# Optimization experiments

Hardware: AMD Instinct MI355X
Metric: run time of the kernel (lower is better)

## Reference

```python
import jax, jax.numpy as jnp
import numpy as np

N, T, F = 20000, 64, 128          # nodes, time steps, feat_dim
B, K = 8192, 32                   # queries, padded neighbor count
WWIN = 64                         # window_w -> delta table size WWIN+1
DD, MD, HD, HH = 16, 64, 128, 64  # delta_dim, msg_dim, hidden_dim, h_dim
Q = 3 * B                         # (v,s,z) x B node-time aggregations


def _lin(k, i, o):
    k1, k2 = jax.random.split(k)
    w = jax.random.normal(k1, (i, o), jnp.float32) / np.sqrt(i).astype(np.float32)
    b = jax.random.normal(k2, (o,), jnp.float32) * 0.01
    return w, b


def setup_inputs() -> dict:
    key = jax.random.key(0)
    ks = jax.random.split(key, 24)
    x_tensor = jax.random.normal(ks[0], (N, T, F), jnp.float32)
    node_ids = jax.random.randint(ks[1], (Q,), 0, N)
    times = jax.random.randint(ks[2], (Q,), 0, T)
    in_u = jax.random.randint(ks[3], (Q, K), 0, N)
    in_tau = jax.random.randint(ks[4], (Q, K), 0, T)
    in_mask = jax.random.uniform(ks[5], (Q, K)) < 0.5
    out_u = jax.random.randint(ks[6], (Q, K), 0, N)
    out_tau = jax.random.randint(ks[7], (Q, K), 0, T)
    out_mask = jax.random.uniform(ks[8], (Q, K)) < 0.5
    d_norm = jax.random.uniform(ks[9], (B,))
    delta_emb = jax.random.normal(ks[10], (WWIN + 1, DD), jnp.float32) * 0.1
    piw1, pib1 = _lin(ks[11], F + DD, MD)
    piw2, pib2 = _lin(ks[12], MD, MD)
    pow1, pob1 = _lin(ks[13], F + DD, MD)
    pow2, pob2 = _lin(ks[14], MD, MD)
    cw1, cb1 = _lin(ks[15], F + 2 * MD, HD)
    cw2, cb2 = _lin(ks[16], HD, HH)
    sw1, sb1 = _lin(ks[17], 3 * HH + 1, HD)
    sw2, sb2 = _lin(ks[18], HD, 1)
    return dict(x_tensor=x_tensor, d_norm=d_norm, delta_emb=delta_emb,
                piw1=piw1, pib1=pib1, piw2=piw2, pib2=pib2,
                pow1=pow1, pob1=pob1, pow2=pow2, pob2=pob2,
                cw1=cw1, cb1=cb1, cw2=cw2, cb2=cb2,
                sw1=sw1, sb1=sb1, sw2=sw2, sb2=sb2,
                node_ids=node_ids, times=times,
                in_u=in_u, in_tau=in_tau, in_mask=in_mask,
                out_u=out_u, out_tau=out_tau, out_mask=out_mask)


def reference(x_tensor, d_norm, delta_emb,
              piw1, pib1, piw2, pib2,
              pow1, pob1, pow2, pob2,
              cw1, cb1, cw2, cb2,
              sw1, sb1, sw2, sb2,
              node_ids, times, in_u, in_tau, in_mask, out_u, out_tau, out_mask):
    def mlp2(x, w1, b1, w2, b2):  # Linear -> ReLU -> Linear
        return jnp.maximum(x @ w1 + b1, 0.0) @ w2 + b2

    def agg(u, tau, mask, sign, w1, b1, w2, b2):
        # sign=+1: in arcs delta = clamp(t - tau); sign=-1: out arcs delta = clamp(tau - t)
        delta = jnp.clip(sign * (times[:, None] - tau), 0, WWIN)     # [Q,K]
        x_u = x_tensor[u, tau]                                        # [Q,K,F] gather
        msg = mlp2(jnp.concatenate([x_u, delta_emb[delta]], -1), w1, b1, w2, b2)  # [Q,K,MD]
        m = mask[..., None].astype(msg.dtype)
        return (msg * m).sum(1) / jnp.maximum(m.sum(1), 1.0)         # masked mean; empty -> zeros

    m_in = agg(in_u, in_tau, in_mask, 1, piw1, pib1, piw2, pib2)
    m_out = agg(out_u, out_tau, out_mask, -1, pow1, pob1, pow2, pob2)
    x_vt = x_tensor[node_ids, times]                                  # [Q,F]
    # combine: Linear -> ReLU -> (Dropout eval) -> Linear -> ReLU
    h = jnp.maximum(mlp2(jnp.concatenate([x_vt, m_in, m_out], -1), cw1, cb1, cw2, cb2), 0.0)  # [Q,HH]
    feat = jnp.concatenate([h.reshape(B, 3 * HH), d_norm[:, None]], -1)  # [B, 3*HH+1]
    return mlp2(feat, sw1, sb1, sw2, sb2)[:, 0]                       # [B]
```

## Files before the change

kernel.cpp:

```cpp
#include <hip/hip_runtime.h>
#include <hip/hip_bf16.h>

#define NND   20000
#define TSTEP 64
#define FF    128
#define BB    8192
#define KK    32
#define QQ    (3*BB)
#define WWINC 64
#define DDIM  16
#define MDIM  64
#define HDIM  128
#define HHDIM 64

typedef __attribute__((ext_vector_type(8)))  short short8;
typedef __attribute__((ext_vector_type(16))) float f32x16;

union FragU { unsigned u[4]; short8 s; };

static __device__ __forceinline__ unsigned pkbf(float a, float b) {
    union { float f; unsigned u; } ua, ub; ua.f = a; ub.f = b;
    unsigned ra = (ua.u + 0x7FFFu + ((ua.u >> 16) & 1u)) >> 16;
    unsigned rb = (ub.u + 0x7FFFu + ((ub.u >> 16) & 1u)) >> 16;
    return (ra & 0xFFFFu) | (rb << 16);
}
static __device__ __forceinline__ short f2bf(float a) {
    union { float f; unsigned u; } v; v.f = a;
    return (short)((v.u + 0x7FFFu + ((v.u >> 16) & 1u)) >> 16);
}

__global__ void pack_kernel(const float* __restrict__ cw1, const float* __restrict__ cw2,
                            const float* __restrict__ sw1,
                            short* __restrict__ cw1f, short* __restrict__ cw2f,
                            short* __restrict__ sw1f)
{
    const int gid = blockIdx.x * 256 + threadIdx.x;
    const int ln  = gid & 63;
    const int f   = gid >> 6;
    const int kr8 = 8 * (ln >> 5);
    const int c   = ln & 31;
    FragU v;
    if (f < 64) {
        const int s = f >> 2, n = f & 3;
        #pragma unroll
        for (int i = 0; i < 8; i += 2)
            v.u[i >> 1] = pkbf(cw1[(16*s + kr8 + i)     * HDIM + 32*n + c],
                               cw1[(16*s + kr8 + i + 1) * HDIM + 32*n + c]);
        *(short8*)&cw1f[f * 512 + ln * 8] = v.s;
    } else if (f < 80) {
        const int f2 = f - 64, s = f2 >> 1, n = f2 & 1;
        #pragma unroll
        for (int i = 0; i < 8; i += 2)
            v.u[i >> 1] = pkbf(cw2[(16*s + kr8 + i)     * HHDIM + 32*n + c],
                               cw2[(16*s + kr8 + i + 1) * HHDIM + 32*n + c]);
        *(short8*)&cw2f[f2 * 512 + ln * 8] = v.s;
    } else {
        const int f3 = f - 80, s = f3 >> 2, n = f3 & 3;
        #pragma unroll
        for (int i = 0; i < 8; i += 2)
            v.u[i >> 1] = pkbf(sw1[(16*s + kr8 + i)     * HDIM + 32*n + c],
                               sw1[(16*s + kr8 + i + 1) * HDIM + 32*n + c]);
        *(short8*)&sw1f[f3 * 512 + ln * 8] = v.s;
    }
}

#define NW  4
#define HLD 72

__global__ __launch_bounds__(256, 3)
void agg_mfma_kernel(const float* __restrict__ x, const float* __restrict__ demb,
                     const float* __restrict__ w1, const float* __restrict__ b1,
                     const float* __restrict__ w2, const float* __restrict__ b2,
                     const int* __restrict__ times, const int* __restrict__ uu,
                     const int* __restrict__ tt, const int* __restrict__ mm,
                     float* __restrict__ mout, const int sign, const int nwaves)
{
    __shared__ short w1f[9 * 2 * 64 * 8];
    __shared__ short Hs[NW][KK * HLD];

    const int tid  = threadIdx.x;
    const int lane = tid & 63;
    const int wv   = tid >> 6;
    const int r    = lane & 31;
    const int hi   = lane >> 5;

    for (int f = tid; f < 9 * 2 * 64; f += 256) {
        const int ln = f & 63, sn = f >> 6, s = sn >> 1, n = sn & 1;
        const int krow = 16 * s + 8 * (ln >> 5);
        const int col  = 32 * n + (ln & 31);
        #pragma unroll
        for (int i = 0; i < 8; i += 2) {
            const float va = w1[(krow + i) * MDIM + col];
            const float vb = w1[(krow + i + 1) * MDIM + col];
            *(unsigned*)&w1f[f * 8 + i] = pkbf(va, vb);
        }
    }
    short8 w2f[4][2];
    #pragma unroll
    for (int s = 0; s < 4; s++)
        #pragma unroll
        for (int n = 0; n < 2; n++) {
            FragU fu;
            #pragma unroll
            for (int i = 0; i < 8; i += 2) {
                const float va = w2[(16 * s + 8 * hi + i) * MDIM + 32 * n + r];
                const float vb = w2[(16 * s + 8 * hi + i + 1) * MDIM + 32 * n + r];
                fu.u[i >> 1] = pkbf(va, vb);
            }
            w2f[s][n] = fu.s;
        }
    const float b1c0 = b1[r], b1c1 = b1[32 + r];
    const float b2c0 = b2[r], b2c1 = b2[32 + r];
    __syncthreads();

    const int gwave = blockIdx.x * NW + wv;
    for (int q = gwave; q < QQ; q += nwaves) {
        const int t = times[q];
        int xb = 0, db = 0, mk = 0;
        if (lane < KK) {
            const int u   = uu[q * KK + lane];
            const int tau = tt[q * KK + lane];
            mk = mm[q * KK + lane];
            int d = (sign > 0) ? (t - tau) : (tau - t);
            d = d < 0 ? 0 : (d > WWINC ? WWINC : d);
            xb = u * (TSTEP * FF) + tau * FF;
            db = d * DDIM;
        }
        const unsigned long long bal = __ballot(mk != 0);
        const float cnt  = (float)__popcll(bal);
        const float cinv = 1.0f / fmaxf(cnt, 1.0f);
        const float has  = cnt > 0.0f ? 1.0f : 0.0f;
        const int xbr = __shfl(xb, r, 64);
        const int dbr = __shfl(db, r, 64);
        const int mkr = __shfl(mk, r, 64);

        f32x16 acc0, acc1;
        #pragma unroll
        for (int i = 0; i < 16; i++) { acc0[i] = 0.0f; acc1[i] = 0.0f; }

        const float* xrow = x + xbr + 8 * hi;
        #pragma unroll 4
        for (int s = 0; s < 8; s++) {
            float4 p0 = make_float4(0.f, 0.f, 0.f, 0.f), p1 = p0;
            if (mkr) {
                p0 = *(const float4*)(xrow + 16 * s);
                p1 = *(const float4*)(xrow + 16 * s + 4);
            }
            FragU fa;
            fa.u[0] = pkbf(p0.x, p0.y); fa.u[1] = pkbf(p0.z, p0.w);
            fa.u[2] = pkbf(p1.x, p1.y); fa.u[3] = pkbf(p1.z, p1.w);
            const short8 bf0 = *(const short8*)&w1f[(s * 2 + 0) * 512 + lane * 8];
            const short8 bf1 = *(const short8*)&w1f[(s * 2 + 1) * 512 + lane * 8];
            acc0 = __builtin_amdgcn_mfma_f32_32x32x16_bf16(fa.s, bf0, acc0, 0, 0, 0);
            acc1 = __builtin_amdgcn_mfma_f32_32x32x16_bf16(fa.s, bf1, acc1, 0, 0, 0);
        }
        {
            float4 p0 = make_float4(0.f, 0.f, 0.f, 0.f), p1 = p0;
            if (mkr) {
                p0 = *(const float4*)(demb + dbr + 8 * hi);
                p1 = *(const float4*)(demb + dbr + 8 * hi + 4);
            }
            FragU fa;
            fa.u[0] = pkbf(p0.x, p0.y); fa.u[1] = pkbf(p0.z, p0.w);
            fa.u[2] = pkbf(p1.x, p1.y); fa.u[3] = pkbf(p1.z, p1.w);
            const short8 bf0 = *(const short8*)&w1f[(8 * 2 + 0) * 512 + lane * 8];
            const short8 bf1 = *(const short8*)&w1f[(8 * 2 + 1) * 512 + lane * 8];
            acc0 = __builtin_amdgcn_mfma_f32_32x32x16_bf16(fa.s, bf0, acc0, 0, 0, 0);
            acc1 = __builtin_amdgcn_mfma_f32_32x32x16_bf16(fa.s, bf1, acc1, 0, 0, 0);
        }

        #pragma unroll
        for (int g = 0; g < 16; g++) {
            const int rr = (g & 3) + 8 * (g >> 2) + 4 * hi;
            const float mrow = (float)((bal >> rr) & 1ull);
            const float h0 = fmaxf(acc0[g] + b1c0, 0.0f) * mrow;
            const float h1 = fmaxf(acc1[g] + b1c1, 0.0f) * mrow;
            Hs[wv][rr * HLD + r]      = f2bf(h0);
            Hs[wv][rr * HLD + 32 + r] = f2bf(h1);
        }

        f32x16 c0, c1;
        #pragma unroll
        for (int i = 0; i < 16; i++) { c0[i] = 0.0f; c1[i] = 0.0f; }
        #pragma unroll
        for (int s = 0; s < 4; s++) {
            const short8 a = *(const short8*)&Hs[wv][r * HLD + 16 * s + 8 * hi];
            c0 = __builtin_amdgcn_mfma_f32_32x32x16_bf16(a, w2f[s][0], c0, 0, 0, 0);
            c1 = __builtin_amdgcn_mfma_f32_32x32x16_bf16(a, w2f[s][1], c1, 0, 0, 0);
        }

        float p0s = 0.0f, p1s = 0.0f;
        #pragma unroll
        for (int g = 0; g < 16; g++) { p0s += c0[g]; p1s += c1[g]; }
        p0s += __shfl_xor(p0s, 32, 64);
        p1s += __shfl_xor(p1s, 32, 64);
        const float outv = (hi ? p1s : p0s) * cinv + (hi ? b2c1 : b2c0) * has;
        mout[(size_t)q * MDIM + 32 * hi + r] = outv;
    }
}

#define HLD2 136

__global__ __launch_bounds__(64, 2)
void combine_mfma(const float* __restrict__ x,
                  const int* __restrict__ node_ids, const int* __restrict__ times,
                  const float* __restrict__ min_ws, const float* __restrict__ mout_ws,
                  const short* __restrict__ cw1f, const float* __restrict__ cb1,
                  const short* __restrict__ cw2f, const float* __restrict__ cb2,
                  short* __restrict__ h_bf)
{
    __shared__ short Hs[KK * HLD2];
    const int lane = threadIdx.x & 63;
    const int r = lane & 31, hi = lane >> 5;
    const int qb = blockIdx.x * 32;
    const int q  = qb + r;
    const int xb = node_ids[q] * (TSTEP * FF) + times[q] * FF;

    f32x16 acc[4];
    #pragma unroll
    for (int n = 0; n < 4; n++)
        #pragma unroll
        for (int i = 0; i < 16; i++) acc[n][i] = 0.0f;

    const float* xrow = x + xb + 8 * hi;
    #pragma unroll
    for (int s = 0; s < 8; s++) {
        const float4 p0 = *(const float4*)(xrow + 16 * s);
        const float4 p1 = *(const float4*)(xrow + 16 * s + 4);
        FragU fa;
        fa.u[0] = pkbf(p0.x, p0.y); fa.u[1] = pkbf(p0.z, p0.w);
        fa.u[2] = pkbf(p1.x, p1.y); fa.u[3] = pkbf(p1.z, p1.w);
        #pragma unroll
        for (int n = 0; n < 4; n++) {
            const short8 bf = *(const short8*)&cw1f[(s * 4 + n) * 512 + lane * 8];
            acc[n] = __builtin_amdgcn_mfma_f32_32x32x16_bf16(fa.s, bf, acc[n], 0, 0, 0);
        }
    }
    const float* mrow = min_ws + (size_t)q * MDIM + 8 * hi;
    #pragma unroll
    for (int s = 0; s < 4; s++) {
        const float4 p0 = *(const float4*)(mrow + 16 * s);
        const float4 p1 = *(const float4*)(mrow + 16 * s + 4);
        FragU fa;
        fa.u[0] = pkbf(p0.x, p0.y); fa.u[1] = pkbf(p0.z, p0.w);
        fa.u[2] = pkbf(p1.x, p1.y); fa.u[3] = pkbf(p1.z, p1.w);
        #pragma unroll
        for (int n = 0; n < 4; n++) {
            const short8 bf = *(const short8*)&cw1f[((s + 8) * 4 + n) * 512 + lane * 8];
            acc[n] = __builtin_amdgcn_mfma_f32_32x32x16_bf16(fa.s, bf, acc[n], 0, 0, 0);
        }
    }
    const float* orow = mout_ws + (size_t)q * MDIM + 8 * hi;
    #pragma unroll
    for (int s = 0; s < 4; s++) {
        const float4 p0 = *(const float4*)(orow + 16 * s);
        const float4 p1 = *(const float4*)(orow + 16 * s + 4);
        FragU fa;
        fa.u[0] = pkbf(p0.x, p0.y); fa.u[1] = pkbf(p0.z, p0.w);
        fa.u[2] = pkbf(p1.x, p1.y); fa.u[3] = pkbf(p1.z, p1.w);
        #pragma unroll
        for (int n = 0; n < 4; n++) {
            const short8 bf = *(const short8*)&cw1f[((s + 12) * 4 + n) * 512 + lane * 8];
            acc[n] = __builtin_amdgcn_mfma_f32_32x32x16_bf16(fa.s, bf, acc[n], 0, 0, 0);
        }
    }

    #pragma unroll
    for (int n = 0; n < 4; n++) {
        const float bias = cb1[32 * n + r];
        #pragma unroll
        for (int g = 0; g < 16; g++) {
            const int rr = (g & 3) + 8 * (g >> 2) + 4 * hi;
            Hs[rr * HLD2 + 32 * n + r] = f2bf(fmaxf(acc[n][g] + bias, 0.0f));
        }
    }
    __syncthreads();

    f32x16 c0, c1;
    #pragma unroll
    for (int i = 0; i < 16; i++) { c0[i] = 0.0f; c1[i] = 0.0f; }
    #pragma unroll
    for (int s = 0; s < 8; s++) {
        const short8 a = *(const short8*)&Hs[r * HLD2 + 16 * s + 8 * hi];
        const short8 b0 = *(const short8*)&cw2f[(s * 2 + 0) * 512 + lane * 8];
        const short8 b1v = *(const short8*)&cw2f[(s * 2 + 1) * 512 + lane * 8];
        c0 = __builtin_amdgcn_mfma_f32_32x32x16_bf16(a, b0, c0, 0, 0, 0);
        c1 = __builtin_amdgcn_mfma_f32_32x32x16_bf16(a, b1v, c1, 0, 0, 0);
    }
    const float bb0 = cb2[r], bb1 = cb2[32 + r];
    #pragma unroll
    for (int g = 0; g < 16; g++) {
        const int rr = (g & 3) + 8 * (g >> 2) + 4 * hi;
        h_bf[(size_t)(qb + rr) * HHDIM + r]      = f2bf(fmaxf(c0[g] + bb0, 0.0f));
        h_bf[(size_t)(qb + rr) * HHDIM + 32 + r] = f2bf(fmaxf(c1[g] + bb1, 0.0f));
    }
}

__global__ __launch_bounds__(64, 2)
void score_mfma(const short* __restrict__ h_bf, const float* __restrict__ dnorm,
                const short* __restrict__ sw1f, const float* __restrict__ sw1,
                const float* __restrict__ sb1, const float* __restrict__ sw2,
                const float* __restrict__ sb2, float* __restrict__ out)
{
    const int lane = threadIdx.x & 63;
    const int r = lane & 31, hi = lane >> 5;
    const int bb = blockIdx.x * 32;

    f32x16 acc[4];
    #pragma unroll
    for (int n = 0; n < 4; n++)
        #pragma unroll
        for (int i = 0; i < 16; i++) acc[n][i] = 0.0f;

    const short* arow = h_bf + (size_t)(bb + r) * 192 + 8 * hi;
    #pragma unroll
    for (int s = 0; s < 12; s++) {
        const short8 a = *(const short8*)(arow + 16 * s);
        #pragma unroll
        for (int n = 0; n < 4; n++) {
            const short8 bf = *(const short8*)&sw1f[(s * 4 + n) * 512 + lane * 8];
            acc[n] = __builtin_amdgcn_mfma_f32_32x32x16_bf16(a, bf, acc[n], 0, 0, 0);
        }
    }

    float sb1c[4], swr[4], sw2c[4];
    #pragma unroll
    for (int n = 0; n < 4; n++) {
        sb1c[n] = sb1[32 * n + r];
        swr[n]  = sw1[192 * HDIM + 32 * n + r];
        sw2c[n] = sw2[32 * n + r];
    }
    const float sb2v = sb2[0];

    #pragma unroll
    for (int g = 0; g < 16; g++) {
        const int rr = (g & 3) + 8 * (g >> 2) + 4 * hi;
        const float dn = dnorm[bb + rr];
        float p = 0.0f;
        #pragma unroll
        for (int n = 0; n < 4; n++)
            p += fmaxf(acc[n][g] + sb1c[n] + dn * swr[n], 0.0f) * sw2c[n];
        p += __shfl_xor(p, 1);  p += __shfl_xor(p, 2);  p += __shfl_xor(p, 4);
        p += __shfl_xor(p, 8);  p += __shfl_xor(p, 16);
        if (r == 0) out[bb + rr] = p + sb2v;
    }
}

extern "C" void kernel_launch(void* const* d_in, const int* in_sizes, int n_in,
                              void* d_out, int out_size, void* d_ws, size_t ws_size,
                              hipStream_t stream)
{
    const float* x     = (const float*)d_in[0];
    const float* dnorm = (const float*)d_in[1];
    const float* demb  = (const float*)d_in[2];
    const float* piw1  = (const float*)d_in[3];
    const float* pib1  = (const float*)d_in[4];
    const float* piw2  = (const float*)d_in[5];
    const float* pib2  = (const float*)d_in[6];
    const float* pow1  = (const float*)d_in[7];
    const float* pob1  = (const float*)d_in[8];
    const float* pow2  = (const float*)d_in[9];
    const float* pob2  = (const float*)d_in[10];
    const float* cw1   = (const float*)d_in[11];
    const float* cb1   = (const float*)d_in[12];
    const float* cw2   = (const float*)d_in[13];
    const float* cb2   = (const float*)d_in[14];
    const float* sw1   = (const float*)d_in[15];
    const float* sb1   = (const float*)d_in[16];
    const float* sw2   = (const float*)d_in[17];
    const float* sb2   = (const float*)d_in[18];
    const int* node_ids = (const int*)d_in[19];
    const int* times    = (const int*)d_in[20];
    const int* in_u     = (const int*)d_in[21];
    const int* in_tau   = (const int*)d_in[22];
    const int* in_mask  = (const int*)d_in[23];
    const int* out_u    = (const int*)d_in[24];
    const int* out_tau  = (const int*)d_in[25];
    const int* out_mask = (const int*)d_in[26];

    float* ws      = (float*)d_ws;
    float* min_ws  = ws;
    float* mout_ws = ws + (size_t)QQ * MDIM;
    short* h_bf    = (short*)(ws + (size_t)2 * QQ * MDIM);
    short* wpack   = (short*)(ws + (size_t)2 * QQ * MDIM + (size_t)BB * 192 / 2);
    short* cw1f    = wpack;
    short* cw2f    = wpack + 32768;
    short* sw1f    = wpack + 40960;
    float* out     = (float*)d_out;

    const int grid = 768;
    const int nwaves = grid * NW;

    pack_kernel<<<32, 256, 0, stream>>>(cw1, cw2, sw1, cw1f, cw2f, sw1f);
    agg_mfma_kernel<<<grid, 256, 0, stream>>>(x, demb, piw1, pib1, piw2, pib2,
                                              times, in_u, in_tau, in_mask,
                                              min_ws, 1, nwaves);
    agg_mfma_kernel<<<grid, 256, 0, stream>>>(x, demb, pow1, pob1, pow2, pob2,
                                              times, out_u, out_tau, out_mask,
                                              mout_ws, -1, nwaves);
    combine_mfma<<<QQ / 32, 64, 0, stream>>>(x, node_ids, times, min_ws, mout_ws,
                                             cw1f, cb1, cw2f, cb2, h_bf);
    score_mfma<<<BB / 32, 64, 0, stream>>>(h_bf, dnorm, sw1f, sw1, sb1, sw2, sb2, out);
}
```

Measured before the change: 920.5 us.

## Fuse in/out aggregation kernels and hoist second MLP layer past masked mean

Merges the two per-direction aggregation launches into one grid, with each half of the blocks selecting its own weights and indices. Because the second linear layer is affine, the masked mean is now taken over the ReLU hidden activations first. The second layer then runs once per query, batched as a 32-row MFMA across queries in the block, instead of once per neighbor. Also prefetches the next query's indices and raises the occupancy hint. In exchange it hardcodes exactly 8 queries per wave, and the block-level sync plus the 2-of-4-wave epilogue leaves some waves idle.

After: 919.7 us. No clear change (-0.1%).

```diff
diff --git a/kernel.cpp b/kernel.cpp
--- a/kernel.cpp
+++ b/kernel.cpp
@@ -64,19 +64,38 @@
     }
 }
 
-#define NW  4
-#define HLD 72
-
-__global__ __launch_bounds__(256, 3)
-void agg_mfma_kernel(const float* __restrict__ x, const float* __restrict__ demb,
-                     const float* __restrict__ w1, const float* __restrict__ b1,
-                     const float* __restrict__ w2, const float* __restrict__ b2,
-                     const int* __restrict__ times, const int* __restrict__ uu,
-                     const int* __restrict__ tt, const int* __restrict__ mm,
-                     float* __restrict__ mout, const int sign, const int nwaves)
+#define NW     4
+#define AGRID  768
+#define NWAVES (AGRID * NW)
+#define MLD    72
+
+__global__ __launch_bounds__(256, 4)
+void agg_fused_kernel(const float* __restrict__ x, const float* __restrict__ demb,
+                      const float* __restrict__ piw1, const float* __restrict__ pib1,
+                      const float* __restrict__ piw2, const float* __restrict__ pib2,
+                      const float* __restrict__ pow1, const float* __restrict__ pob1,
+                      const float* __restrict__ pow2, const float* __restrict__ pob2,
+                      const int* __restrict__ times,
+                      const int* __restrict__ iu, const int* __restrict__ it, const int* __restrict__ im,
+                      const int* __restrict__ ou, const int* __restrict__ ot, const int* __restrict__ om,
+                      float* __restrict__ min_ws, float* __restrict__ mout_ws)
 {
     __shared__ short w1f[9 * 2 * 64 * 8];
-    __shared__ short Hs[NW][KK * HLD];
+    __shared__ short meanb[32 * MLD];
+    __shared__ int   qidxL[32];
+    __shared__ float hasL[32];
+
+    const int half = (blockIdx.x >= AGRID) ? 1 : 0;
+    const int bid  = blockIdx.x - half * AGRID;
+    const float* w1 = half ? pow1 : piw1;
+    const float* b1 = half ? pob1 : pib1;
+    const float* w2 = half ? pow2 : piw2;
+    const float* b2 = half ? pob2 : pib2;
+    const int* uu = half ? ou : iu;
+    const int* tt = half ? ot : it;
+    const int* mm = half ? om : im;
+    float* mo = half ? mout_ws : min_ws;
+    const int sg = half ? -1 : 1;
 
     const int tid  = threadIdx.x;
     const int lane = tid & 63;
@@ -95,37 +114,39 @@
             *(unsigned*)&w1f[f * 8 + i] = pkbf(va, vb);
         }
     }
-    short8 w2f[4][2];
-    #pragma unroll
-    for (int s = 0; s < 4; s++)
-        #pragma unroll
-        for (int n = 0; n < 2; n++) {
-            FragU fu;
-            #pragma unroll
-            for (int i = 0; i < 8; i += 2) {
-                const float va = w2[(16 * s + 8 * hi + i) * MDIM + 32 * n + r];
-                const float vb = w2[(16 * s + 8 * hi + i + 1) * MDIM + 32 * n + r];
-                fu.u[i >> 1] = pkbf(va, vb);
+    const float b1c0 = b1[r], b1c1 = b1[32 + r];
+    __syncthreads();
+
+    const int gwave = bid * NW + wv;
+    int q = gwave;
+
+    int pu = 0, ptau = 0, pmk = 0;
+    if (lane < KK) {
+        pu   = uu[q * KK + lane];
+        ptau = tt[q * KK + lane];
+        pmk  = mm[q * KK + lane];
+    }
+    int ptq = times[q];
+
+    for (int qi = 0; qi < 8; qi++) {
+        const int t   = ptq;
+        const int mk  = pmk;
+        int d = sg * (t - ptau);
+        d = d < 0 ? 0 : (d > WWINC ? WWINC : d);
+        const int xb = pu * (TSTEP * FF) + ptau * FF;
+        const int db = d * DDIM;
+        const int qcur = q;
+
+        if (qi < 7) {
+            q += NWAVES;
+            if (lane < KK) {
+                pu   = uu[q * KK + lane];
+                ptau = tt[q * KK + lane];
+                pmk  = mm[q * KK + lane];
             }
-            w2f[s][n] = fu.s;
-        }
-    const float b1c0 = b1[r], b1c1 = b1[32 + r];
-    const float b2c0 = b2[r], b2c1 = b2[32 + r];
-    __syncthreads();
-
-    const int gwave = blockIdx.x * NW + wv;
-    for (int q = gwave; q < QQ; q += nwaves) {
-        const int t = times[q];
-        int xb = 0, db = 0, mk = 0;
-        if (lane < KK) {
-            const int u   = uu[q * KK + lane];
-            const int tau = tt[q * KK + lane];
-            mk = mm[q * KK + lane];
-            int d = (sign > 0) ? (t - tau) : (tau - t);
-            d = d < 0 ? 0 : (d > WWINC ? WWINC : d);
-            xb = u * (TSTEP * FF) + tau * FF;
-            db = d * DDIM;
-        }
+            ptq = times[q];
+        }
+
         const unsigned long long bal = __ballot(mk != 0);
         const float cnt  = (float)__popcll(bal);
         const float cinv = 1.0f / fmaxf(cnt, 1.0f);
@@ -169,33 +190,45 @@
             acc1 = __builtin_amdgcn_mfma_f32_32x32x16_bf16(fa.s, bf1, acc1, 0, 0, 0);
         }
 
+        float s0 = 0.0f, s1 = 0.0f;
         #pragma unroll
         for (int g = 0; g < 16; g++) {
             const int rr = (g & 3) + 8 * (g >> 2) + 4 * hi;
             const float mrow = (float)((bal >> rr) & 1ull);
-            const float h0 = fmaxf(acc0[g] + b1c0, 0.0f) * mrow;
-            const float h1 = fmaxf(acc1[g] + b1c1, 0.0f) * mrow;
-            Hs[wv][rr * HLD + r]      = f2bf(h0);
-            Hs[wv][rr * HLD + 32 + r] = f2bf(h1);
-        }
-
-        f32x16 c0, c1;
-        #pragma unroll
-        for (int i = 0; i < 16; i++) { c0[i] = 0.0f; c1[i] = 0.0f; }
+            s0 = fmaf(fmaxf(acc0[g] + b1c0, 0.0f), mrow, s0);
+            s1 = fmaf(fmaxf(acc1[g] + b1c1, 0.0f), mrow, s1);
+        }
+        s0 += __shfl_xor(s0, 32, 64);
+        s1 += __shfl_xor(s1, 32, 64);
+        const int row = wv * 8 + qi;
+        meanb[row * MLD + lane] = f2bf((hi ? s1 : s0) * cinv);
+        if (lane == 0) { qidxL[row] = qcur; hasL[row] = has; }
+    }
+
+    __syncthreads();
+
+    if (wv < 2) {
+        f32x16 c;
+        #pragma unroll
+        for (int i = 0; i < 16; i++) c[i] = 0.0f;
         #pragma unroll
         for (int s = 0; s < 4; s++) {
-            const short8 a = *(const short8*)&Hs[wv][r * HLD + 16 * s + 8 * hi];
-            c0 = __builtin_amdgcn_mfma_f32_32x32x16_bf16(a, w2f[s][0], c0, 0, 0, 0);
-            c1 = __builtin_amdgcn_mfma_f32_32x32x16_bf16(a, w2f[s][1], c1, 0, 0, 0);
-        }
-
-        float p0s = 0.0f, p1s = 0.0f;
-        #pragma unroll
-        for (int g = 0; g < 16; g++) { p0s += c0[g]; p1s += c1[g]; }
-        p0s += __shfl_xor(p0s, 32, 64);
-        p1s += __shfl_xor(p1s, 32, 64);
-        const float outv = (hi ? p1s : p0s) * cinv + (hi ? b2c1 : b2c0) * has;
-        mout[(size_t)q * MDIM + 32 * hi + r] = outv;
+            FragU fb;
+            #pragma unroll
+            for (int i = 0; i < 8; i += 2) {
+                const float va = w2[(16 * s + 8 * hi + i)     * MDIM + 32 * wv + r];
+                const float vb = w2[(16 * s + 8 * hi + i + 1) * MDIM + 32 * wv + r];
+                fb.u[i >> 1] = pkbf(va, vb);
+            }
+            const short8 a = *(const short8*)&meanb[r * MLD + 16 * s + 8 * hi];
+            c = __builtin_amdgcn_mfma_f32_32x32x16_bf16(a, fb.s, c, 0, 0, 0);
+        }
+        const float b2c = b2[32 * wv + r];
+        #pragma unroll
+        for (int g = 0; g < 16; g++) {
+            const int rr = (g & 3) + 8 * (g >> 2) + 4 * hi;
+            mo[(size_t)qidxL[rr] * MDIM + 32 * wv + r] = c[g] + b2c * hasL[rr];
+        }
     }
 }
 
@@ -388,16 +421,14 @@
     short* sw1f    = wpack + 40960;
     float* out     = (float*)d_out;
 
-    const int grid = 768;
-    const int nwaves = grid * NW;
-
     pack_kernel<<<32, 256, 0, stream>>>(cw1, cw2, sw1, cw1f, cw2f, sw1f);
-    agg_mfma_kernel<<<grid, 256, 0, stream>>>(x, demb, piw1, pib1, piw2, pib2,
-                                              times, in_u, in_tau, in_mask,
-                                              min_ws, 1, nwaves);
-    agg_mfma_kernel<<<grid, 256, 0, stream>>>(x, demb, pow1, pob1, pow2, pob2,
-                                              times, out_u, out_tau, out_mask,
-                                              mout_ws, -1, nwaves);
+    agg_fused_kernel<<<2 * AGRID, 256, 0, stream>>>(x, demb,
+                                                    piw1, pib1, piw2, pib2,
+                                                    pow1, pob1, pow2, pob2,
+                                                    times,
+                                                    in_u, in_tau, in_mask,
+                                                    out_u, out_tau, out_mask,
+                                                    min_ws, mout_ws);
     combine_mfma<<<QQ / 32, 64, 0, stream>>>(x, node_ids, times, min_ws, mout_ws,
                                              cw1f, cb1, cw2f, cb2, h_bf);
     score_mfma<<<BB / 32, 64, 0, stream>>>(h_bf, dnorm, sw1f, sw1, sb1, sw2, sb2, out);
```
